# Optimization experiments

Hardware: AMD Instinct MI355X
Metric: run time of the kernel (lower is better)

## Reference

```python
import jax, jax.numpy as jnp
import numpy as np

SOM = (32, 32)   # som_dim; SOM[0]*SOM[1] == num_embeddings
LR = 0.05


def setup_inputs() -> dict:
    key = jax.random.key(0)
    k1, k2 = jax.random.split(key)
    B, K, D = 65536, 1024, 256
    x = jax.random.normal(k1, (B, D), dtype=jnp.float32)
    embeddings = jax.random.uniform(k2, (K, D), dtype=jnp.float32)  # torch.rand init
    return {"x": x, "embeddings": embeddings}


def reference(x, embeddings):
    K, D = embeddings.shape
    # pairwise squared distances: [B, K]
    dist = (jnp.sum(x * x, axis=1, keepdims=True)
            + jnp.sum(embeddings * embeddings, axis=1)
            - 2.0 * (x @ embeddings.T))
    n_min = jnp.argmin(dist, axis=1)          # [B]
    z_q = embeddings[n_min]                   # [B, D]

    # SOM grid coordinates and clamped neighbors
    n_x = n_min // SOM[1]
    n_y = n_min % SOM[1]
    x_up = jnp.where(n_x < SOM[0] - 1, n_x + 1, n_x)
    x_down = jnp.where(n_x > 0, n_x - 1, n_x)
    y_right = jnp.where(n_y < SOM[1] - 1, n_y + 1, n_y)
    y_left = jnp.where(n_y > 0, n_y - 1, n_y)
    idx_up = x_up * SOM[1] + n_y
    idx_down = x_down * SOM[1] + n_y
    idx_right = n_x * SOM[1] + y_right
    idx_left = n_x * SOM[1] + y_left

    # [B, 4, D] neighbor gather (order: up, down, left, right as in torch code)
    nbr_idx = jnp.stack([idx_up, idx_down, idx_left, idx_right], axis=1)
    z_q_neighbors = embeddings[nbr_idx]

    # SOM scatter update (torch does one-hot matmuls; segment_sum is the fused form)
    dw = x - z_q                              # [B, D]
    seg = lambda idx: jax.ops.segment_sum(dw, idx, num_segments=K)
    new_embeddings = jax.lax.stop_gradient(
        embeddings
        + LR * seg(n_min)
        + 0.5 * LR * (seg(idx_up) + seg(idx_down) + seg(idx_right) + seg(idx_left))
    )

    commit_loss = jnp.mean((x - z_q) ** 2)
    som_loss = jnp.mean((jax.lax.stop_gradient(x)[:, None, :] - z_q_neighbors) ** 2)
    return z_q, commit_loss, som_loss, new_embeddings
```

## Files before the change

### kernel.cpp

```cpp
#include <hip/hip_runtime.h>

#define B_ROWS 65536
#define DDIM   256
#define KEMB   1024
#define LRC    0.05f
#define BM 64
#define BN 128

typedef __attribute__((ext_vector_type(8))) _Float16 half8;
typedef __attribute__((ext_vector_type(4))) float f32x4;

#define SX_OFF    0u
#define CNT_OFF   1048576u
#define SUMS_OFF  1052672u
#define ESQ_OFF   1053312u
#define CUR_OFF   1057408u
#define NMIN_OFF  1061504u
#define ROWS_OFF  1585792u
#define EH_OFF    1847936u

static __device__ __forceinline__ unsigned short f2h(float f) {
  _Float16 h = (_Float16)f;
  return *(unsigned short*)&h;
}
static __device__ __forceinline__ float h2f(unsigned short u) {
  _Float16 h = *(_Float16*)&u;
  return (float)h;
}
static __device__ __forceinline__ void glds16(const void* g, void* l) {
  __builtin_amdgcn_global_load_lds(
      (const __attribute__((address_space(1))) unsigned int*)g,
      (__attribute__((address_space(3))) unsigned int*)l, 16, 0, 0);
}

__global__ __launch_bounds__(256) void convert_kernel(
    const float* __restrict__ X, const float* __restrict__ E,
    unsigned short* __restrict__ outU, unsigned short* __restrict__ Eh,
    float* __restrict__ esq, double* __restrict__ sums) {
  __shared__ float red[256];
  const size_t nX8 = (size_t)B_ROWS * DDIM / 8;
  size_t i = (size_t)blockIdx.x * 256 + threadIdx.x;
  bool isX = (i < nX8);
  const float* src;
  unsigned short *dh, *dl = nullptr;
  if (isX) {
    size_t off = i * 8;
    src = X + off;
    dh = outU + (off >> 8) * 512 + (off & 255);
    dl = dh + 256;
  } else {
    size_t off = (i - nX8) * 8;
    src = E + off;
    dh = Eh + off;
  }
  const float4 v0 = *(const float4*)src;
  const float4 v1 = *(const float4*)(src + 4);
  float f[8] = {v0.x, v0.y, v0.z, v0.w, v1.x, v1.y, v1.z, v1.w};
  unsigned short h[8], l[8];
  float part = 0.f;
#pragma unroll
  for (int j = 0; j < 8; ++j) {
    h[j] = f2h(f[j]);
    l[j] = f2h(f[j] - h2f(h[j]));
    part += f[j] * f[j];
  }
  *(uint4*)dh = *(const uint4*)h;
  if (isX) *(uint4*)dl = *(const uint4*)l;
  if (!isX) {
    float s = part;
    for (int off = 16; off > 0; off >>= 1) s += __shfl_down(s, off, 32);
    if ((threadIdx.x & 31) == 0) esq[(i - nX8) >> 5] = s;
  }
  red[threadIdx.x] = isX ? part : 0.f;
  __syncthreads();
  for (int s = 128; s > 0; s >>= 1) {
    if (threadIdx.x < s) red[threadIdx.x] += red[threadIdx.x + s];
    __syncthreads();
  }
  if (threadIdx.x == 0 && isX)
    atomicAdd(&sums[8 + ((int)blockIdx.x & 63)], (double)red[0]);
}

__global__ __launch_bounds__(256, 2) void gemm_argmin_kernel(
    const unsigned short* __restrict__ XhlU, const unsigned short* __restrict__ EhW,
    const float* __restrict__ esq, const float* __restrict__ Ef,
    int* __restrict__ nmin, int* __restrict__ counts, float* __restrict__ zq) {
  __shared__ __align__(16) unsigned short sX[2][8][256][8];
  __shared__ __align__(16) unsigned short sE[2][512][8];

  const int tid  = threadIdx.x;
  const int lane = tid & 63, w = tid >> 6;
  const int lrow = lane & 15;
  const int qidx = lane >> 4;
  const int rowbase = (w >> 1) * 32;
  const int colb    = (w & 1) * 64;
  const int bm0 = (int)blockIdx.x * BM;

  int ec_row[2], ec_q8[2];
#pragma unroll
  for (int j = 0; j < 2; ++j) {
    const int c = j * 256 + tid;
    ec_row[j] = c >> 2;
    ec_q8[j]  = ((c & 3) ^ ((ec_row[j] >> 1) & 3)) * 8;
  }

#pragma unroll
  for (int j = 0; j < 2; ++j)
    glds16(EhW + (size_t)ec_row[j] * DDIM + ec_q8[j], (char*)&sE[0][j * 256 + tid][0]);
#pragma unroll
  for (int it = 0; it < 16; ++it) {
    const int c    = it * 256 + tid;
    const int tile = c >> 11;
    const int kcc  = (c >> 8) & 7;
    const int cc   = c & 255;
    const int row  = cc >> 2;
    const int q    = (cc & 3) ^ ((row >> 1) & 3);
    glds16(XhlU + (size_t)(bm0 + row) * 512 + tile * 256 + kcc * 32 + q * 8,
           (char*)sX + (size_t)c * 16);
  }

  float rbest[8];
  int   ridx[8];
#pragma unroll
  for (int i = 0; i < 8; ++i) { rbest[i] = 3.4e38f; ridx[i] = 0; }

  int ra[2], rb[4];
#pragma unroll
  for (int t = 0; t < 2; ++t) {
    const int m = rowbase + t * 16 + lrow;
    ra[t] = (m << 2) | (qidx ^ ((m >> 1) & 3));
  }
#pragma unroll
  for (int t = 0; t < 4; ++t) {
    const int n = colb + t * 16 + lrow;
    rb[t] = (n << 2) | (qidx ^ ((n >> 1) & 3));
  }

  __syncthreads();

  for (int nt = 0; nt < 8; ++nt) {
    f32x4 acc[2][4];
#pragma unroll
    for (int i = 0; i < 2; ++i)
#pragma unroll
      for (int j = 0; j < 4; ++j) acc[i][j] = (f32x4){0.f, 0.f, 0.f, 0.f};

#pragma unroll
    for (int kcc = 0; kcc < 8; ++kcc) {
      const int s   = nt * 8 + kcc;
      const int cur = s & 1;
      if (s < 63) {
        const int ns = s + 1;
        const int nnt = ns >> 3, nk = ns & 7;
#pragma unroll
        for (int j = 0; j < 2; ++j) {
          const int c = j * 256 + tid;
          glds16(EhW + (size_t)(nnt * BN + ec_row[j]) * DDIM + nk * 32 + ec_q8[j],
                 (char*)&sE[cur ^ 1][c][0]);
        }
      }
      half8 af0[2], af1[2], bfr[4];
#pragma unroll
      for (int t = 0; t < 2; ++t) {
        af0[t] = *(const half8*)&sX[0][kcc][ra[t]][0];
        af1[t] = *(const half8*)&sX[1][kcc][ra[t]][0];
      }
#pragma unroll
      for (int t = 0; t < 4; ++t) bfr[t] = *(const half8*)&sE[cur][rb[t]][0];
#pragma unroll
      for (int tr = 0; tr < 2; ++tr)
#pragma unroll
        for (int tc = 0; tc < 4; ++tc)
          acc[tr][tc] = __builtin_amdgcn_mfma_f32_16x16x32_f16(
              af0[tr], bfr[tc], acc[tr][tc], 0, 0, 0);
#pragma unroll
      for (int tr = 0; tr < 2; ++tr)
#pragma unroll
        for (int tc = 0; tc < 4; ++tc)
          acc[tr][tc] = __builtin_amdgcn_mfma_f32_16x16x32_f16(
              af1[tr], bfr[tc], acc[tr][tc], 0, 0, 0);
      __syncthreads();
    }
#pragma unroll
    for (int tc = 0; tc < 4; ++tc) {
      const int col = nt * BN + colb + tc * 16 + lrow;
      const float eq = esq[col];
#pragma unroll
      for (int tr = 0; tr < 2; ++tr)
#pragma unroll
        for (int rr = 0; rr < 4; ++rr) {
          float d = eq - 2.0f * acc[tr][tc][rr];
          const int slot = tr * 4 + rr;
          if (d < rbest[slot]) { rbest[slot] = d; ridx[slot] = col; }
        }
    }
  }

  float* cdd = (float*)&sE[0][0][0];
  int*   cdi = (int*)(cdd + 128);
  int*   snm = cdi + 128;
  int*   h   = (int*)&sX[0][0][0][0];

#pragma unroll
  for (int i = 0; i < 4; ++i) h[tid + i * 256] = 0;

#pragma unroll
  for (int slot = 0; slot < 8; ++slot) {
    float bd = rbest[slot];
    int   bi = ridx[slot];
#pragma unroll
    for (int off = 1; off < 16; off <<= 1) {
      float od = __shfl_xor(bd, off, 64);
      int   oi = __shfl_xor(bi, off, 64);
      if (od < bd || (od == bd && oi < bi)) { bd = od; bi = oi; }
    }
    if (lrow == 0) {
      const int row = rowbase + (slot >> 2) * 16 + (lane >> 4) * 4 + (slot & 3);
      cdd[(w & 1) * 64 + row] = bd;
      cdi[(w & 1) * 64 + row] = bi;
    }
  }
  __syncthreads();
  if (tid < BM) {
    float d0 = cdd[tid], d1 = cdd[64 + tid];
    int   i0 = cdi[tid], i1 = cdi[64 + tid];
    int bi = (d1 < d0 || (d1 == d0 && i1 < i0)) ? i1 : i0;
    nmin[bm0 + tid] = bi;
    snm[tid] = bi;
    atomicAdd(&h[bi], 1);
  }
  __syncthreads();
#pragma unroll
  for (int i = 0; i < 4; ++i) {
    int v = h[tid + i * 256];
    if (v) atomicAdd(&counts[tid + i * 256], v);
  }
  const int r0 = w * 16;
#pragma unroll 4
  for (int r = 0; r < 16; ++r) {
    const int k = snm[r0 + r];
    const float4 v = *(const float4*)(Ef + (size_t)k * DDIM + lane * 4);
    *(float4*)(zq + (size_t)(bm0 + r0 + r) * DDIM + lane * 4) = v;
  }
}

__global__ __launch_bounds__(1024) void scan_kernel(
    const int* __restrict__ counts, int* __restrict__ cur) {
  __shared__ int tmp[KEMB];
  int tid = threadIdx.x;
  int v = counts[tid];
  tmp[tid] = v;
  __syncthreads();
  for (int off = 1; off < 1024; off <<= 1) {
    int u = (tid >= off) ? tmp[tid - off] : 0;
    __syncthreads();
    tmp[tid] += u;
    __syncthreads();
  }
  cur[tid] = tmp[tid] - v;
}

__global__ __launch_bounds__(1024) void scatter_kernel(
    const int* __restrict__ nm, int* __restrict__ cur,
    int* __restrict__ rows) {
  __shared__ int lcnt[KEMB], lbase[KEMB], lrank[KEMB];
  int tid = threadIdx.x;
  lcnt[tid] = 0; lrank[tid] = 0;
  __syncthreads();
  int b = blockIdx.x * 1024 + tid;
  int k = nm[b];
  atomicAdd(&lcnt[k], 1);
  __syncthreads();
  if (lcnt[tid] > 0) lbase[tid] = atomicAdd(&cur[tid], lcnt[tid]);
  __syncthreads();
  int r = atomicAdd(&lrank[k], 1);
  rows[lbase[k] + r] = b;
}

__global__ __launch_bounds__(256) void sxsum_kernel(
    const int* __restrict__ rows, const int* __restrict__ nm,
    const float* __restrict__ X, float* __restrict__ SX) {
  __shared__ int sb[64], sk[64];
  int tid = threadIdx.x;
  int p0 = blockIdx.x * 64;
  if (tid < 64) sb[tid] = rows[p0 + tid];
  __syncthreads();
  if (tid < 64) sk[tid] = nm[sb[tid]];
  __syncthreads();
  float acc = 0.f;
  int kprev = sk[0];
  for (int i = 0; i < 64; ++i) {
    int k = sk[i];
    if (k != kprev) {
      atomicAdd(&SX[(size_t)kprev * DDIM + tid], acc);
      acc = 0.f;
      kprev = k;
    }
    acc += X[(size_t)sb[i] * DDIM + tid];
  }
  atomicAdd(&SX[(size_t)kprev * DDIM + tid], acc);
}

__global__ __launch_bounds__(256) void stencil_kernel(
    const float* __restrict__ E, const float* __restrict__ SX,
    const int* __restrict__ counts, const float* __restrict__ esq,
    double* __restrict__ sums, float* __restrict__ out) {
  __shared__ float redc[256], reds[256];
  int k = blockIdx.x, t = threadIdx.x;
  int kx = k >> 5, ky = k & 31;
  int j1 = (kx >= 1)  ? k - 32 : k;
  int j2 = (kx <= 30) ? k + 32 : k;
  int j3 = (ky >= 1)  ? k - 1  : k;
  int j4 = (ky <= 30) ? k + 1  : k;
  int fU = (kx < 31) ? k + 32 : k;
  int fD = (kx > 0)  ? k - 32 : k;
  int fL = (ky > 0)  ? k - 1  : k;
  int fR = (ky < 31) ? k + 1  : k;

  float e   = E[(size_t)k * DDIM + t];
  float sxk = SX[(size_t)k * DDIM + t];
  float Tk = sxk - (float)counts[k] * e;
  float T1 = SX[(size_t)j1 * DDIM + t] - (float)counts[j1] * E[(size_t)j1 * DDIM + t];
  float T2 = SX[(size_t)j2 * DDIM + t] - (float)counts[j2] * E[(size_t)j2 * DDIM + t];
  float T3 = SX[(size_t)j3 * DDIM + t] - (float)counts[j3] * E[(size_t)j3 * DDIM + t];
  float T4 = SX[(size_t)j4 * DDIM + t] - (float)counts[j4] * E[(size_t)j4 * DDIM + t];
  float v = e + LRC * Tk + 0.5f * LRC * (T1 + T2 + T3 + T4);
  out[(size_t)B_ROWS * DDIM + 2 + (size_t)k * DDIM + t] = v;

  float eU = E[(size_t)fU * DDIM + t], eD = E[(size_t)fD * DDIM + t];
  float eL = E[(size_t)fL * DDIM + t], eR = E[(size_t)fR * DDIM + t];
  float cp = -2.f * sxk * e;
  float sp = -2.f * sxk * (eU + eD + eL + eR);
  if (t == 0) {
    float ck = (float)counts[k];
    cp += ck * esq[k];
    sp += ck * (esq[fU] + esq[fD] + esq[fL] + esq[fR]);
  }
  redc[t] = cp; reds[t] = sp;
  __syncthreads();
  for (int s = 128; s > 0; s >>= 1) {
    if (t < s) { redc[t] += redc[t + s]; reds[t] += reds[t + s]; }
    __syncthreads();
  }
  if (t == 0) {
    atomicAdd(&sums[1], (double)redc[0]);
    atomicAdd(&sums[2], (double)reds[0]);
  }
}

__global__ void finalize_kernel(const double* __restrict__ sums,
                                float* __restrict__ out) {
  double xsq = 0.0;
  for (int s = 0; s < 64; ++s) xsq += sums[8 + s];
  out[(size_t)B_ROWS * DDIM]     = (float)((xsq + sums[1]) / ((double)B_ROWS * DDIM));
  out[(size_t)B_ROWS * DDIM + 1] =
      (float)((4.0 * xsq + sums[2]) / ((double)B_ROWS * 4.0 * DDIM));
}

extern "C" void kernel_launch(void* const* d_in, const int* in_sizes, int n_in,
                              void* d_out, int out_size, void* d_ws, size_t ws_size,
                              hipStream_t stream) {
  const float* X = (const float*)d_in[0];
  const float* E = (const float*)d_in[1];
  float* out = (float*)d_out;
  unsigned short* outU = (unsigned short*)d_out;
  char* ws = (char*)d_ws;

  float*          SX   = (float*)(ws + SX_OFF);
  int*            cnts = (int*)(ws + CNT_OFF);
  double*         sums = (double*)(ws + SUMS_OFF);
  float*          esq  = (float*)(ws + ESQ_OFF);
  int*            cur  = (int*)(ws + CUR_OFF);
  int*            nm   = (int*)(ws + NMIN_OFF);
  int*            rows = (int*)(ws + ROWS_OFF);
  unsigned short* EhW  = (unsigned short*)(ws + EH_OFF);

  hipMemsetAsync(ws, 0, ESQ_OFF, stream);

  convert_kernel<<<(B_ROWS * (DDIM / 8) + KEMB * (DDIM / 8)) / 256, 256, 0, stream>>>(
      X, E, outU, EhW, esq, sums);
  gemm_argmin_kernel<<<B_ROWS / BM, 256, 0, stream>>>(outU, EhW, esq, E, nm, cnts, out);
  scan_kernel<<<1, 1024, 0, stream>>>(cnts, cur);
  scatter_kernel<<<B_ROWS / 1024, 1024, 0, stream>>>(nm, cur, rows);
  sxsum_kernel<<<B_ROWS / 64, 256, 0, stream>>>(rows, nm, X, SX);
  stencil_kernel<<<KEMB, 256, 0, stream>>>(E, SX, cnts, esq, sums, out);
  finalize_kernel<<<1, 1, 0, stream>>>(sums, out);
}
```

Baseline: 281.9 us.

## Fuse X fp16 hi/lo split into GEMM and read E fragments from global

The fp16 hi/lo split of X and the x-squared partial sums move out of the separate convert kernel and into the GEMM prologue, which reads fp32 X directly into swizzled shared memory. This removes a full write and reread of the split X buffer through the output area. The GEMM also drops the double-buffered shared-memory staging of E and its per-step barriers, loading B fragments straight from global or L2, since the 512 KB fp16 codebook is heavily reused across blocks. The sxsum kernel chunk size is halved so more blocks run, which trades parallelism for more atomics.

```diff
diff --git a/kernel.cpp b/kernel.cpp
--- a/kernel.cpp
+++ b/kernel.cpp
@@ -27,66 +27,34 @@
   _Float16 h = *(_Float16*)&u;
   return (float)h;
 }
-static __device__ __forceinline__ void glds16(const void* g, void* l) {
-  __builtin_amdgcn_global_load_lds(
-      (const __attribute__((address_space(1))) unsigned int*)g,
-      (__attribute__((address_space(3))) unsigned int*)l, 16, 0, 0);
-}
 
 __global__ __launch_bounds__(256) void convert_kernel(
-    const float* __restrict__ X, const float* __restrict__ E,
-    unsigned short* __restrict__ outU, unsigned short* __restrict__ Eh,
-    float* __restrict__ esq, double* __restrict__ sums) {
-  __shared__ float red[256];
-  const size_t nX8 = (size_t)B_ROWS * DDIM / 8;
+    const float* __restrict__ E, unsigned short* __restrict__ Eh,
+    float* __restrict__ esq) {
   size_t i = (size_t)blockIdx.x * 256 + threadIdx.x;
-  bool isX = (i < nX8);
-  const float* src;
-  unsigned short *dh, *dl = nullptr;
-  if (isX) {
-    size_t off = i * 8;
-    src = X + off;
-    dh = outU + (off >> 8) * 512 + (off & 255);
-    dl = dh + 256;
-  } else {
-    size_t off = (i - nX8) * 8;
-    src = E + off;
-    dh = Eh + off;
-  }
-  const float4 v0 = *(const float4*)src;
-  const float4 v1 = *(const float4*)(src + 4);
+  size_t off = i * 8;
+  const float4 v0 = *(const float4*)(E + off);
+  const float4 v1 = *(const float4*)(E + off + 4);
   float f[8] = {v0.x, v0.y, v0.z, v0.w, v1.x, v1.y, v1.z, v1.w};
-  unsigned short h[8], l[8];
+  unsigned short h[8];
   float part = 0.f;
 #pragma unroll
   for (int j = 0; j < 8; ++j) {
     h[j] = f2h(f[j]);
-    l[j] = f2h(f[j] - h2f(h[j]));
     part += f[j] * f[j];
   }
-  *(uint4*)dh = *(const uint4*)h;
-  if (isX) *(uint4*)dl = *(const uint4*)l;
-  if (!isX) {
-    float s = part;
-    for (int off = 16; off > 0; off >>= 1) s += __shfl_down(s, off, 32);
-    if ((threadIdx.x & 31) == 0) esq[(i - nX8) >> 5] = s;
-  }
-  red[threadIdx.x] = isX ? part : 0.f;
-  __syncthreads();
-  for (int s = 128; s > 0; s >>= 1) {
-    if (threadIdx.x < s) red[threadIdx.x] += red[threadIdx.x + s];
-    __syncthreads();
-  }
-  if (threadIdx.x == 0 && isX)
-    atomicAdd(&sums[8 + ((int)blockIdx.x & 63)], (double)red[0]);
+  *(uint4*)(Eh + off) = *(const uint4*)h;
+  float s = part;
+  for (int o = 16; o > 0; o >>= 1) s += __shfl_down(s, o, 32);
+  if ((threadIdx.x & 31) == 0) esq[i >> 5] = s;
 }
 
 __global__ __launch_bounds__(256, 2) void gemm_argmin_kernel(
-    const unsigned short* __restrict__ XhlU, const unsigned short* __restrict__ EhW,
+    const float* __restrict__ X, const unsigned short* __restrict__ EhW,
     const float* __restrict__ esq, const float* __restrict__ Ef,
-    int* __restrict__ nmin, int* __restrict__ counts, float* __restrict__ zq) {
+    int* __restrict__ nmin, int* __restrict__ counts, float* __restrict__ zq,
+    double* __restrict__ sums) {
   __shared__ __align__(16) unsigned short sX[2][8][256][8];
-  __shared__ __align__(16) unsigned short sE[2][512][8];
 
   const int tid  = threadIdx.x;
   const int lane = tid & 63, w = tid >> 6;
@@ -96,27 +64,31 @@
   const int colb    = (w & 1) * 64;
   const int bm0 = (int)blockIdx.x * BM;
 
-  int ec_row[2], ec_q8[2];
-#pragma unroll
-  for (int j = 0; j < 2; ++j) {
-    const int c = j * 256 + tid;
-    ec_row[j] = c >> 2;
-    ec_q8[j]  = ((c & 3) ^ ((ec_row[j] >> 1) & 3)) * 8;
-  }
-
-#pragma unroll
-  for (int j = 0; j < 2; ++j)
-    glds16(EhW + (size_t)ec_row[j] * DDIM + ec_q8[j], (char*)&sE[0][j * 256 + tid][0]);
-#pragma unroll
-  for (int it = 0; it < 16; ++it) {
-    const int c    = it * 256 + tid;
-    const int tile = c >> 11;
-    const int kcc  = (c >> 8) & 7;
-    const int cc   = c & 255;
-    const int row  = cc >> 2;
-    const int q    = (cc & 3) ^ ((row >> 1) & 3);
-    glds16(XhlU + (size_t)(bm0 + row) * 512 + tile * 256 + kcc * 32 + q * 8,
-           (char*)sX + (size_t)c * 16);
+  {
+    const int row = tid >> 2, p = tid & 3;
+    const float* xp = X + (size_t)(bm0 + row) * DDIM + p * 64;
+    float part = 0.f;
+#pragma unroll
+    for (int j = 0; j < 8; ++j) {
+      const float4 a = *(const float4*)(xp + j * 8);
+      const float4 b = *(const float4*)(xp + j * 8 + 4);
+      float f[8] = {a.x, a.y, a.z, a.w, b.x, b.y, b.z, b.w};
+      unsigned short hh[8], ll[8];
+#pragma unroll
+      for (int m = 0; m < 8; ++m) {
+        hh[m] = f2h(f[m]);
+        ll[m] = f2h(f[m] - h2f(hh[m]));
+        part += f[m] * f[m];
+      }
+      const int kcc = p * 2 + (j >> 2);
+      const int ch  = (row << 2) | ((j & 3) ^ ((row >> 1) & 3));
+      *(uint4*)&sX[0][kcc][ch][0] = *(const uint4*)hh;
+      *(uint4*)&sX[1][kcc][ch][0] = *(const uint4*)ll;
+    }
+#pragma unroll
+    for (int o = 32; o > 0; o >>= 1) part += __shfl_down(part, o);
+    if (lane == 0)
+      atomicAdd(&sums[8 + (((int)blockIdx.x * 4 + w) & 63)], (double)part);
   }
 
   float rbest[8];
@@ -124,17 +96,16 @@
 #pragma unroll
   for (int i = 0; i < 8; ++i) { rbest[i] = 3.4e38f; ridx[i] = 0; }
 
-  int ra[2], rb[4];
+  int ra[2];
 #pragma unroll
   for (int t = 0; t < 2; ++t) {
     const int m = rowbase + t * 16 + lrow;
     ra[t] = (m << 2) | (qidx ^ ((m >> 1) & 3));
   }
-#pragma unroll
-  for (int t = 0; t < 4; ++t) {
-    const int n = colb + t * 16 + lrow;
-    rb[t] = (n << 2) | (qidx ^ ((n >> 1) & 3));
-  }
+  const unsigned short* bp[4];
+#pragma unroll
+  for (int t = 0; t < 4; ++t)
+    bp[t] = EhW + (size_t)(colb + t * 16 + lrow) * DDIM + qidx * 8;
 
   __syncthreads();
 
@@ -145,29 +116,19 @@
 #pragma unroll
       for (int j = 0; j < 4; ++j) acc[i][j] = (f32x4){0.f, 0.f, 0.f, 0.f};
 
+    const size_t ntoff = (size_t)nt * BN * DDIM;
 #pragma unroll
     for (int kcc = 0; kcc < 8; ++kcc) {
-      const int s   = nt * 8 + kcc;
-      const int cur = s & 1;
-      if (s < 63) {
-        const int ns = s + 1;
-        const int nnt = ns >> 3, nk = ns & 7;
-#pragma unroll
-        for (int j = 0; j < 2; ++j) {
-          const int c = j * 256 + tid;
-          glds16(EhW + (size_t)(nnt * BN + ec_row[j]) * DDIM + nk * 32 + ec_q8[j],
-                 (char*)&sE[cur ^ 1][c][0]);
-        }
-      }
       half8 af0[2], af1[2], bfr[4];
+#pragma unroll
+      for (int t = 0; t < 4; ++t)
+        bfr[t] = *(const half8*)(bp[t] + ntoff + kcc * 32);
 #pragma unroll
       for (int t = 0; t < 2; ++t) {
         af0[t] = *(const half8*)&sX[0][kcc][ra[t]][0];
         af1[t] = *(const half8*)&sX[1][kcc][ra[t]][0];
       }
 #pragma unroll
-      for (int t = 0; t < 4; ++t) bfr[t] = *(const half8*)&sE[cur][rb[t]][0];
-#pragma unroll
       for (int tr = 0; tr < 2; ++tr)
 #pragma unroll
         for (int tc = 0; tc < 4; ++tc)
@@ -179,7 +140,6 @@
         for (int tc = 0; tc < 4; ++tc)
           acc[tr][tc] = __builtin_amdgcn_mfma_f32_16x16x32_f16(
               af1[tr], bfr[tc], acc[tr][tc], 0, 0, 0);
-      __syncthreads();
     }
 #pragma unroll
     for (int tc = 0; tc < 4; ++tc) {
@@ -196,10 +156,11 @@
     }
   }
 
-  float* cdd = (float*)&sE[0][0][0];
+  __syncthreads();
+  float* cdd = (float*)&sX[0][0][0][0];
   int*   cdi = (int*)(cdd + 128);
   int*   snm = cdi + 128;
-  int*   h   = (int*)&sX[0][0][0][0];
+  int*   h   = snm + 64;
 
 #pragma unroll
   for (int i = 0; i < 4; ++i) h[tid + i * 256] = 0;
@@ -280,16 +241,16 @@
 __global__ __launch_bounds__(256) void sxsum_kernel(
     const int* __restrict__ rows, const int* __restrict__ nm,
     const float* __restrict__ X, float* __restrict__ SX) {
-  __shared__ int sb[64], sk[64];
+  __shared__ int sb[32], sk[32];
   int tid = threadIdx.x;
-  int p0 = blockIdx.x * 64;
-  if (tid < 64) sb[tid] = rows[p0 + tid];
-  __syncthreads();
-  if (tid < 64) sk[tid] = nm[sb[tid]];
+  int p0 = blockIdx.x * 32;
+  if (tid < 32) sb[tid] = rows[p0 + tid];
+  __syncthreads();
+  if (tid < 32) sk[tid] = nm[sb[tid]];
   __syncthreads();
   float acc = 0.f;
   int kprev = sk[0];
-  for (int i = 0; i < 64; ++i) {
+  for (int i = 0; i < 32; ++i) {
     int k = sk[i];
     if (k != kprev) {
       atomicAdd(&SX[(size_t)kprev * DDIM + tid], acc);
@@ -363,7 +324,6 @@
   const float* X = (const float*)d_in[0];
   const float* E = (const float*)d_in[1];
   float* out = (float*)d_out;
-  unsigned short* outU = (unsigned short*)d_out;
   char* ws = (char*)d_ws;
 
   float*          SX   = (float*)(ws + SX_OFF);
@@ -377,12 +337,12 @@
 
   hipMemsetAsync(ws, 0, ESQ_OFF, stream);
 
-  convert_kernel<<<(B_ROWS * (DDIM / 8) + KEMB * (DDIM / 8)) / 256, 256, 0, stream>>>(
-      X, E, outU, EhW, esq, sums);
-  gemm_argmin_kernel<<<B_ROWS / BM, 256, 0, stream>>>(outU, EhW, esq, E, nm, cnts, out);
+  convert_kernel<<<KEMB * (DDIM / 8) / 256, 256, 0, stream>>>(E, EhW, esq);
+  gemm_argmin_kernel<<<B_ROWS / BM, 256, 0, stream>>>(X, EhW, esq, E, nm, cnts, out,
+                                                      sums);
   scan_kernel<<<1, 1024, 0, stream>>>(cnts, cur);
   scatter_kernel<<<B_ROWS / 1024, 1024, 0, stream>>>(nm, cur, rows);
-  sxsum_kernel<<<B_ROWS / 64, 256, 0, stream>>>(rows, nm, X, SX);
+  sxsum_kernel<<<B_ROWS / 32, 256, 0, stream>>>(rows, nm, X, SX);
   stencil_kernel<<<KEMB, 256, 0, stream>>>(E, SX, cnts, esq, sums, out);
   finalize_kernel<<<1, 1, 0, stream>>>(sums, out);
 }
```

Measured after the change: 298.7 us. +6.0%, slower.
